# Optimization experiments

Hardware: AMD Instinct MI355X
Metric: run time of the kernel (lower is better)

The kernel has to match this reference:

```python
import jax, jax.numpy as jnp
import numpy as np

S_DIM, I_DIM, O_DIM = 1024, 2048, 1024
TOTAL = S_DIM + I_DIM + O_DIM  # 4096
INPUT_DIM, NUM_CLASSES, BATCH = 2048, 1000, 256


def setup_inputs() -> dict:
    key = jax.random.key(0)
    ks = jax.random.split(key, 6)
    x = jax.random.normal(ks[0], (BATCH, INPUT_DIM), dtype=jnp.float32)
    W = jax.random.normal(ks[1], (TOTAL, TOTAL), dtype=jnp.float32) * 0.02
    # torch Linear: weight [out, in], bias [out]
    in_w = jax.random.normal(ks[2], (S_DIM, INPUT_DIM), dtype=jnp.float32) * (1.0 / np.sqrt(INPUT_DIM))
    in_b = jax.random.normal(ks[3], (S_DIM,), dtype=jnp.float32) * 0.01
    out_w = jax.random.normal(ks[4], (NUM_CLASSES, O_DIM), dtype=jnp.float32) * (1.0 / np.sqrt(O_DIM))
    out_b = jax.random.normal(ks[5], (NUM_CLASSES,), dtype=jnp.float32) * 0.01
    return {"x": x, "W": W, "in_w": in_w, "in_b": in_b, "out_w": out_w, "out_b": out_b, "time_steps": 10}


def reference(x, W, in_w, in_b, out_w, out_b, time_steps):
    B = x.shape[0]
    S, I, O = S_DIM, I_DIM, O_DIM
    # slice effective W into 9 sub-blocks (use_lora=False -> W_eff = W)
    W_ss, W_sr, W_so = W[:S, :S], W[:S, S:S + I], W[:S, S + I:]
    W_rs, W_rr, W_ro = W[S:S + I, :S], W[S:S + I, S:S + I], W[S:S + I, S + I:]
    W_os, W_or, W_oo = W[S + I:, :S], W[S + I:, S:S + I], W[S + I:, S + I:]

    E = x @ in_w.T + in_b  # [B, S]
    gate = (jnp.arange(time_steps) % 5 == 0).astype(x.dtype)  # E injected when t%5==0

    init = (jnp.zeros((B, S), x.dtype), jnp.zeros((B, I), x.dtype), jnp.zeros((B, O), x.dtype))

    def step(carry, g):
        Ss, Is, Os = carry
        S_next = jax.nn.relu(Ss @ W_ss + g * E + Is @ W_rs + Os @ W_os)
        I_next = jax.nn.relu(Is @ W_rr + Ss @ W_sr + Os @ W_or)
        O_next = jax.nn.relu(Os @ W_oo + Is @ W_ro + Ss @ W_so)
        return (S_next, I_next, O_next), None

    (Ss, Is, Os), _ = jax.lax.scan(step, init, gate)
    return Os @ out_w.T + out_b  # [B, num_classes]
```

## Files before the change

kernel.cpp:

```cpp
#include <hip/hip_runtime.h>


typedef __bf16 bf16x8 __attribute__((ext_vector_type(8)));
typedef float  f32x16 __attribute__((ext_vector_type(16)));

#define TOTAL 4096
#define BATCH 256
#define INDIM 2048
#define SDIM  1024
#define NCLS  1000

#define MFMA(a, b, c) __builtin_amdgcn_mfma_f32_32x32x16_bf16((a), (b), (c), 0, 0, 0)

__device__ inline f32x16 zero16() {
    f32x16 v;
#pragma unroll
    for (int i = 0; i < 16; ++i) v[i] = 0.f;
    return v;
}

__device__ inline void swz_slot(const float* __restrict__ in, __bf16* __restrict__ out,
                                int C, int Rvalid, int t) {
    const int lane = t & 63;
    const int frag = t >> 6;
    const int kcN = C >> 4;
    const int rt = frag / kcN;
    const int kc = frag - rt * kcN;
    const int r = rt * 32 + (lane & 31);
    const int c = kc * 16 + (lane >> 5) * 8;
    alignas(16) __bf16 v[8];
    if (r < Rvalid) {
        const float* p = in + (size_t)r * C + c;
#pragma unroll
        for (int j = 0; j < 8; ++j) v[j] = (__bf16)p[j];
    } else {
#pragma unroll
        for (int j = 0; j < 8; ++j) v[j] = (__bf16)0.f;
    }
    *(ulonglong2*)(out + (size_t)t * 8) = *(const ulonglong2*)v;
}

__global__ __launch_bounds__(256) void k_prep(const float* __restrict__ W,
                                              const float* __restrict__ x,
                                              const float* __restrict__ in_w,
                                              const float* __restrict__ out_w,
                                              __bf16* __restrict__ WT,
                                              __bf16* __restrict__ XT,
                                              __bf16* __restrict__ IWT,
                                              __bf16* __restrict__ OWT) {
    const int bid = blockIdx.x;
    const int tid = threadIdx.x;
    if (bid < 4096) {
        __shared__ float t[64][65];
        const int n0 = (bid & 63) * 64;
        const int k0 = (bid >> 6) * 64;
        const int x64 = tid & 63;
        const int y = tid >> 6;
#pragma unroll
        for (int r = y; r < 64; r += 4)
            t[r][x64] = W[(size_t)(k0 + r) * TOTAL + (n0 + x64)];
        __syncthreads();
#pragma unroll
        for (int s = tid; s < 512; s += 256) {
            const int frag = s >> 6;
            const int lane = s & 63;
            const int lrt = frag >> 2;
            const int lkc = frag & 3;
            const int r_local = lrt * 32 + (lane & 31);
            const int c_local = lkc * 16 + (lane >> 5) * 8;
            alignas(16) __bf16 v[8];
#pragma unroll
            for (int j = 0; j < 8; ++j) v[j] = (__bf16)t[c_local + j][r_local];
            const size_t fragG = (size_t)((n0 >> 5) + lrt) * (TOTAL / 16) + ((k0 >> 4) + lkc);
            *(ulonglong2*)(WT + fragG * 512 + lane * 8) = *(const ulonglong2*)v;
        }
    } else if (bid < 4352) {
        swz_slot(x, XT, INDIM, BATCH, (bid - 4096) * 256 + tid);
    } else if (bid < 5376) {
        swz_slot(in_w, IWT, INDIM, SDIM, (bid - 4352) * 256 + tid);
    } else {
        swz_slot(out_w, OWT, 1024, NCLS, (bid - 5376) * 256 + tid);
    }
}

__global__ __launch_bounds__(512, 4) void k_gemm_E(const __bf16* __restrict__ xt,
                                                   const __bf16* __restrict__ iwt,
                                                   const float* __restrict__ in_b,
                                                   float* __restrict__ E,
                                                   __bf16* __restrict__ h0) {
    __shared__ float red[8][1024];
    const int wave = threadIdx.x >> 6;
    const int lane = threadIdx.x & 63;
    const int mt = blockIdx.x >> 5;
    const int nt = blockIdx.x & 31;
    const int m0 = mt * 32, n0 = nt * 32;
    const int kc0 = wave * 16;
    const bf16x8* Ap = (const bf16x8*)xt  + ((size_t)mt * (INDIM / 16) + kc0) * 64 + lane;
    const bf16x8* Bp = (const bf16x8*)iwt + ((size_t)nt * (INDIM / 16) + kc0) * 64 + lane;
    f32x16 acc = zero16();
#pragma unroll 4
    for (int i = 0; i < 16; ++i)
        acc = MFMA(Ap[i * 64], Bp[i * 64], acc);
#pragma unroll
    for (int r = 0; r < 16; ++r) {
        int row = (r & 3) + 8 * (r >> 2) + 4 * (lane >> 5);
        red[wave][row * 32 + (lane & 31)] = acc[r];
    }
    __syncthreads();
    const int e0 = threadIdx.x * 2;
    float sx = 0.f, sy = 0.f;
#pragma unroll
    for (int w = 0; w < 8; ++w) {
        float2 v = *(const float2*)&red[w][e0];
        sx += v.x; sy += v.y;
    }
    const int row = e0 >> 5, col = e0 & 31;
    const int m = m0 + row, n = n0 + col;
    float v0 = sx + in_b[n], v1 = sy + in_b[n + 1];
    E[m * SDIM + n]     = v0;
    E[m * SDIM + n + 1] = v1;
    __bf16 o[2];
    o[0] = (__bf16)fmaxf(v0, 0.f);
    o[1] = (__bf16)fmaxf(v1, 0.f);
    const size_t frag = (size_t)(m >> 5) * (TOTAL / 16) + (n >> 4);
    const int lh = (m & 31) + 32 * ((n >> 3) & 1);
    *(uint*)(h0 + frag * 512 + lh * 8 + (n & 7)) = *(const uint*)o;
}

template <int PER>
__device__ inline void step_core(const bf16x8* __restrict__ A0p, const bf16x8* __restrict__ A1p,
                                 const bf16x8* __restrict__ B0p, const bf16x8* __restrict__ B1p,
                                 f32x16& ac0, f32x16& ac1, f32x16& ac2, f32x16& ac3) {
    constexpr int D = 4;
    bf16x8 a0[D], a1[D], b0[D], b1[D];
#pragma unroll
    for (int d = 0; d < D; ++d) {
        const int off = d * 64;
        a0[d] = A0p[off]; a1[d] = A1p[off];
        b0[d] = B0p[off]; b1[d] = B1p[off];
    }
#pragma unroll
    for (int i = 0; i < PER; ++i) {
        const int s = i & (D - 1);
        bf16x8 ca0 = a0[s], ca1 = a1[s], cb0 = b0[s], cb1 = b1[s];
        if (i + D < PER) {
            const int off = (i + D) * 64;
            a0[s] = A0p[off]; a1[s] = A1p[off];
            b0[s] = B0p[off]; b1[s] = B1p[off];
        }
        ac0 = MFMA(ca0, cb0, ac0);
        ac1 = MFMA(ca0, cb1, ac1);
        ac2 = MFMA(ca1, cb0, ac2);
        ac3 = MFMA(ca1, cb1, ac3);
    }
}

template <int CHUNKS>
__global__ __launch_bounds__(512, 2) void k_step(const __bf16* __restrict__ h,
                                                 const __bf16* __restrict__ WT,
                                                 const float* __restrict__ E,
                                                 const int gate,
                                                 __bf16* __restrict__ hn) {
    __shared__ float buf[4][4096];
    const int wave = threadIdx.x >> 6;
    const int lane = threadIdx.x & 63;
    const int mt = blockIdx.x >> 6;
    const int nt = blockIdx.x & 63;
    constexpr int PER = CHUNKS >> 3;
    const int kc0 = wave * PER;

    const bf16x8* A0 = (const bf16x8*)h  + ((size_t)(mt * 2) * (TOTAL / 16) + kc0) * 64 + lane;
    const bf16x8* A1 = A0 + (size_t)(TOTAL / 16) * 64;
    const bf16x8* B0 = (const bf16x8*)WT + ((size_t)(nt * 2) * (TOTAL / 16) + kc0) * 64 + lane;
    const bf16x8* B1 = B0 + (size_t)(TOTAL / 16) * 64;

    f32x16 ac0 = zero16(), ac1 = zero16(), ac2 = zero16(), ac3 = zero16();
    step_core<PER>(A0, A1, B0, B1, ac0, ac1, ac2, ac3);

    f32x16 accs[4] = {ac0, ac1, ac2, ac3};
    if (wave >= 4) {
        float* b = buf[wave - 4];
#pragma unroll
        for (int c = 0; c < 4; ++c)
#pragma unroll
            for (int r = 0; r < 16; ++r)
                b[(c * 16 + r) * 64 + lane] = accs[c][r];
    }
    __syncthreads();
    if (wave < 4) {
        float* b = buf[wave];
#pragma unroll
        for (int c = 0; c < 4; ++c)
#pragma unroll
            for (int r = 0; r < 16; ++r) {
                const int idx = (c * 16 + r) * 64 + lane;
                b[idx] += accs[c][r];
            }
    }
    __syncthreads();

    const int t = threadIdx.x;
    const int c = t >> 7;
    const int r = (t >> 3) & 15;
    const int l0 = (t & 7) * 8;
    const int base = (c * 16 + r) * 64 + l0;
    float4 s0 = {0.f, 0.f, 0.f, 0.f}, s1 = {0.f, 0.f, 0.f, 0.f};
#pragma unroll
    for (int w = 0; w < 4; ++w) {
        const float4* p = (const float4*)&buf[w][base];
        float4 v0 = p[0], v1 = p[1];
        s0.x += v0.x; s0.y += v0.y; s0.z += v0.z; s0.w += v0.w;
        s1.x += v1.x; s1.y += v1.y; s1.z += v1.z; s1.w += v1.w;
    }
    float v[8] = {s0.x, s0.y, s0.z, s0.w, s1.x, s1.y, s1.z, s1.w};
    const int ih = c >> 1, jh = c & 1;
    const int row = ih * 32 + (r & 3) + 8 * (r >> 2) + 4 * (l0 >> 5);
    const int col0 = jh * 32 + (l0 & 31);
    const int m = mt * 64 + row;
    const int n0g = nt * 64 + col0;
    if (gate && n0g < SDIM) {
        const float* Ep = E + m * SDIM + n0g;
#pragma unroll
        for (int j = 0; j < 8; ++j) v[j] += Ep[j];
    }
    alignas(16) __bf16 o[8];
#pragma unroll
    for (int j = 0; j < 8; ++j) o[j] = (__bf16)fmaxf(v[j], 0.f);
    const size_t frag = (size_t)(m >> 5) * (TOTAL / 16) + (n0g >> 4);
    const int lh = (m & 31) + 32 * ((n0g >> 3) & 1);
    *(ulonglong2*)(hn + frag * 512 + lh * 8) = *(const ulonglong2*)o;
}

__global__ __launch_bounds__(512, 4) void k_out(const __bf16* __restrict__ h,
                                                const __bf16* __restrict__ owt,
                                                const float* __restrict__ out_b,
                                                float* __restrict__ out) {
    __shared__ float red[8][1024];
    const int wave = threadIdx.x >> 6;
    const int lane = threadIdx.x & 63;
    const int mt = blockIdx.x >> 5;
    const int ct = blockIdx.x & 31;
    const int m0 = mt * 32, c0 = ct * 32;
    const int kcA0 = (3072 / 16) + wave * 8;
    const int kcB0 = wave * 8;
    const bf16x8* Ap = (const bf16x8*)h   + ((size_t)mt * (TOTAL / 16) + kcA0) * 64 + lane;
    const bf16x8* Bp = (const bf16x8*)owt + ((size_t)ct * (1024 / 16) + kcB0) * 64 + lane;
    f32x16 acc = zero16();
#pragma unroll
    for (int i = 0; i < 8; ++i)
        acc = MFMA(Ap[i * 64], Bp[i * 64], acc);
#pragma unroll
    for (int r = 0; r < 16; ++r) {
        int row = (r & 3) + 8 * (r >> 2) + 4 * (lane >> 5);
        red[wave][row * 32 + (lane & 31)] = acc[r];
    }
    __syncthreads();
    const int e0 = threadIdx.x * 2;
    float sx = 0.f, sy = 0.f;
#pragma unroll
    for (int w = 0; w < 8; ++w) {
        float2 v = *(const float2*)&red[w][e0];
        sx += v.x; sy += v.y;
    }
    const int row = e0 >> 5, col = e0 & 31;
    const int m = m0 + row;
    const int n = c0 + col;
    if (n < NCLS)     out[m * NCLS + n]     = sx + out_b[n];
    if (n + 1 < NCLS) out[m * NCLS + n + 1] = sy + out_b[n + 1];
}

extern "C" void kernel_launch(void* const* d_in, const int* in_sizes, int n_in,
                              void* d_out, int out_size, void* d_ws, size_t ws_size,
                              hipStream_t stream) {
    const float* x     = (const float*)d_in[0];
    const float* W     = (const float*)d_in[1];
    const float* in_w  = (const float*)d_in[2];
    const float* in_b  = (const float*)d_in[3];
    const float* out_w = (const float*)d_in[4];
    const float* out_b = (const float*)d_in[5];
    float* out = (float*)d_out;

    char* ws = (char*)d_ws;
    __bf16* WT  = (__bf16*)(ws + 0);
    __bf16* XT  = (__bf16*)(ws + 33554432);
    __bf16* IWT = (__bf16*)(ws + 34603008);
    __bf16* OWT = (__bf16*)(ws + 38797312);
    float*  Ebuf= (float*)(ws + 40894464);
    __bf16* H0  = (__bf16*)(ws + 41943040);
    __bf16* H1  = (__bf16*)(ws + 44040192);

    k_prep<<<5888, 256, 0, stream>>>(W, x, in_w, out_w, WT, XT, IWT, OWT);

    k_gemm_E<<<256, 512, 0, stream>>>(XT, IWT, in_b, Ebuf, H0);

    const __bf16* hs = H0;
    __bf16* hd = H1;
    for (int t = 1; t < 10; ++t) {
        const int gate = (t % 5 == 0) ? 1 : 0;
        if (t == 1)
            k_step<SDIM / 16><<<256, 512, 0, stream>>>(hs, WT, Ebuf, gate, hd);
        else
            k_step<TOTAL / 16><<<256, 512, 0, stream>>>(hs, WT, Ebuf, gate, hd);
        const __bf16* tmp = hs; hs = hd; hd = (__bf16*)tmp;
    }

    k_out<<<256, 512, 0, stream>>>(hs, OWT, out_b, out);
}
```

Measured before the change: 291.6 us.

## Fuse input projection GEMM into prep kernel reading fp32 directly

The input projection E = x·in_wᵀ + b is computed inside the prep kernel by 256 extra blocks that load fp32 x and in_w directly, convert them to bf16 in registers and run MFMA. This removes the separate swizzle passes for x and in_w and one kernel launch. The W transpose load is widened to float4 reads. The step kernel's explicit register-prefetch pipeline is replaced by a plain unrolled loop, leaving latency hiding to the compiler. The fused E blocks use only 4 waves over K=512 each with uncoalesced per-row loads, so they may run longer than the old dedicated GEMM.

New measurement: 296.8 us. Within noise of the previous version (+1.8%).

```diff
diff --git a/kernel.cpp b/kernel.cpp
--- a/kernel.cpp
+++ b/kernel.cpp
@@ -43,22 +43,26 @@
 __global__ __launch_bounds__(256) void k_prep(const float* __restrict__ W,
                                               const float* __restrict__ x,
                                               const float* __restrict__ in_w,
+                                              const float* __restrict__ in_b,
                                               const float* __restrict__ out_w,
                                               __bf16* __restrict__ WT,
-                                              __bf16* __restrict__ XT,
-                                              __bf16* __restrict__ IWT,
-                                              __bf16* __restrict__ OWT) {
+                                              __bf16* __restrict__ OWT,
+                                              float* __restrict__ Ebuf,
+                                              __bf16* __restrict__ H0) {
+    __shared__ float t[64][65];
     const int bid = blockIdx.x;
     const int tid = threadIdx.x;
     if (bid < 4096) {
-        __shared__ float t[64][65];
         const int n0 = (bid & 63) * 64;
         const int k0 = (bid >> 6) * 64;
-        const int x64 = tid & 63;
-        const int y = tid >> 6;
-#pragma unroll
-        for (int r = y; r < 64; r += 4)
-            t[r][x64] = W[(size_t)(k0 + r) * TOTAL + (n0 + x64)];
+        const int rr = tid >> 4;
+        const int cc = (tid & 15) * 4;
+#pragma unroll
+        for (int p = 0; p < 4; ++p) {
+            const int r = p * 16 + rr;
+            float4 v = *(const float4*)(W + (size_t)(k0 + r) * TOTAL + n0 + cc);
+            t[r][cc] = v.x; t[r][cc + 1] = v.y; t[r][cc + 2] = v.z; t[r][cc + 3] = v.w;
+        }
         __syncthreads();
 #pragma unroll
         for (int s = tid; s < 512; s += 256) {
@@ -75,83 +79,53 @@
             *(ulonglong2*)(WT + fragG * 512 + lane * 8) = *(const ulonglong2*)v;
         }
     } else if (bid < 4352) {
-        swz_slot(x, XT, INDIM, BATCH, (bid - 4096) * 256 + tid);
-    } else if (bid < 5376) {
-        swz_slot(in_w, IWT, INDIM, SDIM, (bid - 4352) * 256 + tid);
+        float* red = &t[0][0];
+        const int eb = bid - 4096;
+        const int mt = eb >> 5, nt = eb & 31;
+        const int wave = tid >> 6, lane = tid & 63;
+        const int l31 = lane & 31, kh = (lane >> 5) * 8;
+        const int k0 = wave * 512;
+        const float* Ax = x    + (size_t)(mt * 32 + l31) * INDIM + k0 + kh;
+        const float* Bw = in_w + (size_t)(nt * 32 + l31) * INDIM + k0 + kh;
+        f32x16 acc = zero16();
+#pragma unroll 4
+        for (int i = 0; i < 32; ++i) {
+            const float* pa = Ax + i * 16;
+            const float* pb = Bw + i * 16;
+            float4 a0 = *(const float4*)pa, a1 = *(const float4*)(pa + 4);
+            float4 b0 = *(const float4*)pb, b1 = *(const float4*)(pb + 4);
+            bf16x8 a, b;
+            a[0] = (__bf16)a0.x; a[1] = (__bf16)a0.y; a[2] = (__bf16)a0.z; a[3] = (__bf16)a0.w;
+            a[4] = (__bf16)a1.x; a[5] = (__bf16)a1.y; a[6] = (__bf16)a1.z; a[7] = (__bf16)a1.w;
+            b[0] = (__bf16)b0.x; b[1] = (__bf16)b0.y; b[2] = (__bf16)b0.z; b[3] = (__bf16)b0.w;
+            b[4] = (__bf16)b1.x; b[5] = (__bf16)b1.y; b[6] = (__bf16)b1.z; b[7] = (__bf16)b1.w;
+            acc = MFMA(a, b, acc);
+        }
+#pragma unroll
+        for (int r = 0; r < 16; ++r) {
+            int row = (r & 3) + 8 * (r >> 2) + 4 * (lane >> 5);
+            red[wave * 1024 + row * 32 + l31] = acc[r];
+        }
+        __syncthreads();
+        const int e0 = tid * 4;
+        float4 s = {0.f, 0.f, 0.f, 0.f};
+#pragma unroll
+        for (int w = 0; w < 4; ++w) {
+            float4 v = *(const float4*)&red[w * 1024 + e0];
+            s.x += v.x; s.y += v.y; s.z += v.z; s.w += v.w;
+        }
+        const int row = e0 >> 5, col = e0 & 31;
+        const int m = mt * 32 + row, n = nt * 32 + col;
+        float v[4] = {s.x + in_b[n], s.y + in_b[n + 1], s.z + in_b[n + 2], s.w + in_b[n + 3]};
+        *(float4*)(Ebuf + m * SDIM + n) = *(const float4*)v;
+        alignas(8) __bf16 o[4];
+#pragma unroll
+        for (int j = 0; j < 4; ++j) o[j] = (__bf16)fmaxf(v[j], 0.f);
+        const size_t frag = (size_t)(m >> 5) * (TOTAL / 16) + (n >> 4);
+        const int lh = (m & 31) + 32 * ((n >> 3) & 1);
+        *(ushort4*)(H0 + frag * 512 + lh * 8 + (n & 7)) = *(const ushort4*)o;
     } else {
-        swz_slot(out_w, OWT, 1024, NCLS, (bid - 5376) * 256 + tid);
-    }
-}
-
-__global__ __launch_bounds__(512, 4) void k_gemm_E(const __bf16* __restrict__ xt,
-                                                   const __bf16* __restrict__ iwt,
-                                                   const float* __restrict__ in_b,
-                                                   float* __restrict__ E,
-                                                   __bf16* __restrict__ h0) {
-    __shared__ float red[8][1024];
-    const int wave = threadIdx.x >> 6;
-    const int lane = threadIdx.x & 63;
-    const int mt = blockIdx.x >> 5;
-    const int nt = blockIdx.x & 31;
-    const int m0 = mt * 32, n0 = nt * 32;
-    const int kc0 = wave * 16;
-    const bf16x8* Ap = (const bf16x8*)xt  + ((size_t)mt * (INDIM / 16) + kc0) * 64 + lane;
-    const bf16x8* Bp = (const bf16x8*)iwt + ((size_t)nt * (INDIM / 16) + kc0) * 64 + lane;
-    f32x16 acc = zero16();
-#pragma unroll 4
-    for (int i = 0; i < 16; ++i)
-        acc = MFMA(Ap[i * 64], Bp[i * 64], acc);
-#pragma unroll
-    for (int r = 0; r < 16; ++r) {
-        int row = (r & 3) + 8 * (r >> 2) + 4 * (lane >> 5);
-        red[wave][row * 32 + (lane & 31)] = acc[r];
-    }
-    __syncthreads();
-    const int e0 = threadIdx.x * 2;
-    float sx = 0.f, sy = 0.f;
-#pragma unroll
-    for (int w = 0; w < 8; ++w) {
-        float2 v = *(const float2*)&red[w][e0];
-        sx += v.x; sy += v.y;
-    }
-    const int row = e0 >> 5, col = e0 & 31;
-    const int m = m0 + row, n = n0 + col;
-    float v0 = sx + in_b[n], v1 = sy + in_b[n + 1];
-    E[m * SDIM + n]     = v0;
-    E[m * SDIM + n + 1] = v1;
-    __bf16 o[2];
-    o[0] = (__bf16)fmaxf(v0, 0.f);
-    o[1] = (__bf16)fmaxf(v1, 0.f);
-    const size_t frag = (size_t)(m >> 5) * (TOTAL / 16) + (n >> 4);
-    const int lh = (m & 31) + 32 * ((n >> 3) & 1);
-    *(uint*)(h0 + frag * 512 + lh * 8 + (n & 7)) = *(const uint*)o;
-}
-
-template <int PER>
-__device__ inline void step_core(const bf16x8* __restrict__ A0p, const bf16x8* __restrict__ A1p,
-                                 const bf16x8* __restrict__ B0p, const bf16x8* __restrict__ B1p,
-                                 f32x16& ac0, f32x16& ac1, f32x16& ac2, f32x16& ac3) {
-    constexpr int D = 4;
-    bf16x8 a0[D], a1[D], b0[D], b1[D];
-#pragma unroll
-    for (int d = 0; d < D; ++d) {
-        const int off = d * 64;
-        a0[d] = A0p[off]; a1[d] = A1p[off];
-        b0[d] = B0p[off]; b1[d] = B1p[off];
-    }
-#pragma unroll
-    for (int i = 0; i < PER; ++i) {
-        const int s = i & (D - 1);
-        bf16x8 ca0 = a0[s], ca1 = a1[s], cb0 = b0[s], cb1 = b1[s];
-        if (i + D < PER) {
-            const int off = (i + D) * 64;
-            a0[s] = A0p[off]; a1[s] = A1p[off];
-            b0[s] = B0p[off]; b1[s] = B1p[off];
-        }
-        ac0 = MFMA(ca0, cb0, ac0);
-        ac1 = MFMA(ca0, cb1, ac1);
-        ac2 = MFMA(ca1, cb0, ac2);
-        ac3 = MFMA(ca1, cb1, ac3);
+        swz_slot(out_w, OWT, 1024, NCLS, (bid - 4352) * 256 + tid);
     }
 }
 
@@ -175,7 +149,18 @@
     const bf16x8* B1 = B0 + (size_t)(TOTAL / 16) * 64;
 
     f32x16 ac0 = zero16(), ac1 = zero16(), ac2 = zero16(), ac3 = zero16();
-    step_core<PER>(A0, A1, B0, B1, ac0, ac1, ac2, ac3);
+#pragma unroll 4
+    for (int i = 0; i < PER; ++i) {
+        const int off = i * 64;
+        bf16x8 a0 = A0[off];
+        bf16x8 a1 = A1[off];
+        bf16x8 b0 = B0[off];
+        bf16x8 b1 = B1[off];
+        ac0 = MFMA(a0, b0, ac0);
+        ac1 = MFMA(a0, b1, ac1);
+        ac2 = MFMA(a1, b0, ac2);
+        ac3 = MFMA(a1, b1, ac3);
+    }
 
     f32x16 accs[4] = {ac0, ac1, ac2, ac3};
     if (wave >= 4) {
@@ -282,16 +267,12 @@
 
     char* ws = (char*)d_ws;
     __bf16* WT  = (__bf16*)(ws + 0);
-    __bf16* XT  = (__bf16*)(ws + 33554432);
-    __bf16* IWT = (__bf16*)(ws + 34603008);
-    __bf16* OWT = (__bf16*)(ws + 38797312);
-    float*  Ebuf= (float*)(ws + 40894464);
-    __bf16* H0  = (__bf16*)(ws + 41943040);
-    __bf16* H1  = (__bf16*)(ws + 44040192);
-
-    k_prep<<<5888, 256, 0, stream>>>(W, x, in_w, out_w, WT, XT, IWT, OWT);
-
-    k_gemm_E<<<256, 512, 0, stream>>>(XT, IWT, in_b, Ebuf, H0);
+    __bf16* OWT = (__bf16*)(ws + 33554432);
+    float*  Ebuf= (float*)(ws + 35651584);
+    __bf16* H0  = (__bf16*)(ws + 36700160);
+    __bf16* H1  = (__bf16*)(ws + 38797312);
+
+    k_prep<<<4864, 256, 0, stream>>>(W, x, in_w, in_b, out_w, WT, OWT, Ebuf, H0);
 
     const __bf16* hs = H0;
     __bf16* hd = H1;
```
